# Kernel optimization log

Measured on AMD Instinct MI355X. Metric: run time of the kernel, lower is better.

Reference implementation:

```python
import jax, jax.numpy as jnp
import numpy as np

B, J, D, T = 4096, 22, 3, 50  # batch, joints, xyz dims, seq_len
N = J * D                     # 66 channels
LW = 3                        # local_window
TAU = 5.0
EPS = 1e-5


def _chain_adj_mask(n):
    m = np.zeros((n, n), dtype=np.float32)
    for i in range(n - 1):
        m[i, i + 1] = 1.0
        m[i + 1, i] = 1.0
    return m


def _band_mask(t, w):
    i = np.arange(t)
    return (np.abs(i[:, None] - i[None, :]) <= w).astype(np.float32)


def setup_inputs() -> dict:
    key = jax.random.key(0)
    ks = jax.random.split(key, 9)
    x = jax.random.normal(ks[0], (B, N, T), dtype=jnp.float32)
    adj = jnp.eye(J, dtype=jnp.float32) + 0.1 * jax.random.normal(ks[1], (J, J), dtype=jnp.float32)
    adj_t = 0.1 * jax.random.normal(ks[2], (T, T), dtype=jnp.float32)
    adj_jc = 0.1 * jax.random.normal(ks[3], (J, D, D), dtype=jnp.float32)
    adj_tj = 0.1 * jax.random.normal(ks[4], (N, T, T), dtype=jnp.float32)
    mlp = jax.random.normal(ks[5], (T, 4), dtype=jnp.float32)
    w_update = 1e-2 * jax.random.normal(ks[6], (T, T), dtype=jnp.float32)
    b_update = jnp.zeros((T,), dtype=jnp.float32)
    alpha = jnp.ones((1, N, 1), dtype=jnp.float32)
    beta = jnp.zeros((1, N, 1), dtype=jnp.float32)
    adj_mask = jnp.asarray(_chain_adj_mask(J))
    traj_mask = jnp.asarray(_band_mask(T, LW))
    u = jax.random.uniform(ks[7], (B, 4), minval=1e-6, maxval=1.0 - 1e-6, dtype=jnp.float32)
    gumbels = -jnp.log(-jnp.log(u))
    return {"x": x, "adj": adj, "adj_t": adj_t, "adj_jc": adj_jc, "adj_tj": adj_tj,
            "mlp": mlp, "w_update": w_update, "b_update": b_update,
            "alpha": alpha, "beta": beta, "adj_mask": adj_mask,
            "traj_mask": traj_mask, "gumbels": gumbels}


def reference(x, adj, adj_t, adj_jc, adj_tj, mlp, w_update, b_update,
              alpha, beta, adj_mask, traj_mask, gumbels):
    xr = x.reshape(B, J, D, T)
    # spatial GC: masked joint-joint adjacency
    x1 = jnp.einsum('vj,bjct->bvct', adj * adj_mask, xr).reshape(B, N, T)
    # temporal GC: banded time-time adjacency shared over channels
    x2 = jnp.einsum('ft,bnt->bnf', adj_t * traj_mask, x)
    # joint-channel GC: per-joint 3x3 channel mixing
    x3 = jnp.einsum('jkc,bjct->bjkt', adj_jc, xr).reshape(B, N, T)
    # spatio-temporal GC: per-channel banded time-time adjacency
    x4 = jnp.einsum('nft,bnt->bnf', adj_tj * traj_mask[None], x)
    # gate: mean-pool over channels -> [B,T] @ [T,4], hard gumbel-softmax
    prob = x.mean(axis=1) @ mlp
    y = jax.nn.softmax((prob + gumbels) / TAU, axis=-1)
    y_hard = jax.nn.one_hot(jnp.argmax(y, axis=-1), 4, dtype=y.dtype)
    gate = y_hard + y - jax.lax.stop_gradient(y)  # straight-through
    # option 0 is zeros, so only options 1..3 contribute
    x_ = (gate[:, 1, None, None] * x2
          + gate[:, 2, None, None] * x3
          + gate[:, 3, None, None] * x4)
    # update linear along time axis
    x_ = (x1 + x_) @ w_update.T + b_update
    # spatial LayerNorm over channel axis
    mean = x_.mean(axis=1, keepdims=True)
    var = ((x_ - mean) ** 2).mean(axis=1, keepdims=True)
    x_ = (x_ - mean) / jnp.sqrt(var + EPS) * alpha + beta
    return x + x_
```

## Files before the change

kernel.cpp:

```cpp
#include <hip/hip_runtime.h>


typedef __attribute__((ext_vector_type(8))) short short8_t;
typedef __attribute__((ext_vector_type(4))) float f32x4_t;

__device__ __forceinline__ unsigned short f2bf(float f) {
    unsigned u = __float_as_uint(f);
    u += 0x7fffu + ((u >> 16) & 1u);
    return (unsigned short)(u >> 16);
}
__device__ __forceinline__ float bf2f(unsigned us) {
    return __uint_as_float(us << 16);
}

#define XLD(nn, tt) (*(const uint2*)((const char*)xbf + (((((nn) << 6) + (tt)) << 1) ^ (((nn) & 7) << 4))))

__global__ __launch_bounds__(256) void pack_kernel(
    const float* __restrict__ adj_t,
    const float* __restrict__ adj_tj,
    unsigned short* __restrict__ ws)
{
    int i = blockIdx.x * 256 + threadIdx.x;
    if (i < 400) {
        int f = i >> 3, j = i & 7;
        int tt = f - 3 + j;
        float v = (j < 7 && tt >= 0 && tt < 50) ? adj_t[f * 50 + tt] : 0.f;
        ws[i] = f2bf(v);
    } else if (i < 26800) {
        int e = i - 400;
        int nf = e >> 3, j = e & 7;
        int f = nf % 50;
        int tt = f - 3 + j;
        float v = (j < 7 && tt >= 0 && tt < 50) ? adj_tj[(size_t)nf * 50 + tt] : 0.f;
        ws[i] = f2bf(v);
    }
}

__global__ __launch_bounds__(256, 2) void dyn_kernel(
    const float* __restrict__ x,
    const float* __restrict__ adj,
    const float* __restrict__ adj_t,
    const float* __restrict__ adj_jc,
    const float* __restrict__ adj_tj,
    const float* __restrict__ mlp,
    const float* __restrict__ w_update,
    const float* __restrict__ alpha,
    const float* __restrict__ beta,
    const float* __restrict__ gumbels,
    const unsigned short* __restrict__ wpack,
    int packed,
    float* __restrict__ out)
{
    __shared__ unsigned short xbf[66 * 64];
    __shared__ float wsum[16];
    __shared__ float as[66], bs[66];

    const int b    = blockIdx.x;
    const int tid  = threadIdx.x;
    const int lane = tid & 63;
    const int wv   = tid >> 6;
    const int li   = lane & 15;
    const int lq   = lane >> 4;
    const int f    = wv * 16 + li;
    const float* __restrict__ xb = x + (size_t)b * 3300;

    const float4 gv = *(const float4*)(gumbels + (size_t)b * 4);

    int sn[4], st0[4], sv[4];
    float cwm[4], cwp[4];
    #pragma unroll
    for (int r = 0; r < 4; ++r) {
        int i = tid + (r << 8);
        if (r == 3 && i > 857) i = 857;
        int n = i / 13, q = i - n * 13;
        sn[r] = n; st0[r] = q * 4;
        int v = n / 3; sv[r] = v;
        cwm[r] = (v > 0)  ? adj[v * 22 + v - 1] : 0.f;
        cwp[r] = (v < 21) ? adj[v * 22 + v + 1] : 0.f;
    }

    short8_t bfrag0, bfrag1;
    #pragma unroll
    for (int j = 0; j < 8; ++j) {
        int k0 = 8 * lq + j;
        int k1 = 32 + 8 * lq + j;
        float v0 = (f < 50) ? w_update[f * 50 + k0] : 0.f;
        float v1 = (f < 50 && k1 < 50) ? w_update[f * 50 + k1] : 0.f;
        bfrag0[j] = (short)f2bf(v0);
        bfrag1[j] = (short)f2bf(v1);
    }

    for (int i = tid; i < 198; i += 256) {
        int n = i / 3, p = i - n * 3;
        int t0 = 52 + p * 4;
        int byteoff = ((n * 64 + t0) * 2) ^ ((n & 7) << 4);
        uint2 z2; z2.x = 0u; z2.y = 0u;
        *(uint2*)((char*)xbf + byteoff) = z2;
    }
    if (tid < 66) { as[tid] = alpha[tid]; bs[tid] = beta[tid]; }

    float2 xa[4], xc[4];
    #pragma unroll
    for (int r = 0; r < 4; ++r) {
        int off = sn[r] * 50 + st0[r];
        xa[r] = *(const float2*)(xb + off);
        int off2 = off + 2; if (off2 > 3298) off2 = 3298;
        xc[r] = *(const float2*)(xb + off2);
    }
    float4 pl = {0.f, 0.f, 0.f, 0.f};
    const float4* __restrict__ mlp4 = (const float4*)mlp;
    #pragma unroll
    for (int r = 0; r < 4; ++r) {
        int n = sn[r], t0 = st0[r];
        bool full = (t0 < 48);
        float v0 = xa[r].x, v1 = xa[r].y;
        float v2 = full ? xc[r].x : 0.f;
        float v3 = full ? xc[r].y : 0.f;
        float4 m0 = mlp4[t0], m1 = mlp4[t0 + 1];
        int i2 = t0 + 2; if (i2 > 49) i2 = 49;
        int i3 = t0 + 3; if (i3 > 49) i3 = 49;
        float4 m2 = mlp4[i2], m3 = mlp4[i3];
        if (r < 3 || tid < 90) {
            pl.x += v0 * m0.x + v1 * m1.x + v2 * m2.x + v3 * m3.x;
            pl.y += v0 * m0.y + v1 * m1.y + v2 * m2.y + v3 * m3.y;
            pl.z += v0 * m0.z + v1 * m1.z + v2 * m2.z + v3 * m3.z;
            pl.w += v0 * m0.w + v1 * m1.w + v2 * m2.w + v3 * m3.w;
        }
        uint2 pk;
        pk.x = (unsigned)f2bf(v0) | ((unsigned)f2bf(v1) << 16);
        pk.y = (unsigned)f2bf(v2) | ((unsigned)f2bf(v3) << 16);
        *(uint2*)((char*)xbf + (((n * 64 + t0) * 2) ^ ((n & 7) << 4))) = pk;
    }
    #pragma unroll
    for (int d = 1; d < 64; d <<= 1) {
        pl.x += __shfl_xor(pl.x, d, 64);
        pl.y += __shfl_xor(pl.y, d, 64);
        pl.z += __shfl_xor(pl.z, d, 64);
        pl.w += __shfl_xor(pl.w, d, 64);
    }
    if (lane == 0) *(float4*)&wsum[wv * 4] = pl;
    __syncthreads();

    int g;
    {
        float4 s0 = *(const float4*)&wsum[0],  s1 = *(const float4*)&wsum[4];
        float4 s2 = *(const float4*)&wsum[8],  s3 = *(const float4*)&wsum[12];
        const float inv = 1.0f / 66.0f;
        float l0 = (s0.x + s1.x + s2.x + s3.x) * inv + gv.x;
        float l1 = (s0.y + s1.y + s2.y + s3.y) * inv + gv.y;
        float l2 = (s0.z + s1.z + s2.z + s3.z) * inv + gv.z;
        float l3 = (s0.w + s1.w + s2.w + s3.w) * inv + gv.w;
        g = 0; float bv = l0;
        if (l1 > bv) { bv = l1; g = 1; }
        if (l2 > bv) { bv = l2; g = 2; }
        if (l3 > bv) { bv = l3; g = 3; }
    }

    uint2 zpk[4];
    if (g == 1 || g == 3) {
        uint4 w0[4], w1[4];
        auto loadrows = [&](int r, uint4* dst) {
            if (packed) {
                const uint4* wt4 = (const uint4*)
                    ((g == 1) ? wpack : wpack + 400 + (size_t)sn[r] * 400);
                #pragma unroll
                for (int k = 0; k < 4; ++k) {
                    int ff = st0[r] + k; if (ff > 49) ff = 49;
                    dst[k] = wt4[ff];
                }
            } else {
                const float* rb = (g == 1) ? adj_t : (adj_tj + (size_t)sn[r] * 2500);
                #pragma unroll
                for (int k = 0; k < 4; ++k) {
                    int ff = st0[r] + k; if (ff > 49) ff = 49;
                    float w[8];
                    #pragma unroll
                    for (int j = 0; j < 8; ++j) {
                        int tt = ff - 3 + j;
                        w[j] = (j < 7 && tt >= 0 && tt < 50) ? rb[ff * 50 + tt] : 0.f;
                    }
                    uint4 u;
                    u.x = (unsigned)f2bf(w[0]) | ((unsigned)f2bf(w[1]) << 16);
                    u.y = (unsigned)f2bf(w[2]) | ((unsigned)f2bf(w[3]) << 16);
                    u.z = (unsigned)f2bf(w[4]) | ((unsigned)f2bf(w[5]) << 16);
                    u.w = (unsigned)f2bf(w[6]) | ((unsigned)f2bf(w[7]) << 16);
                    dst[k] = u;
                }
            }
        };
        loadrows(0, w0);
        #pragma unroll
        for (int r = 0; r < 4; ++r) {
            uint4* wcur = (r & 1) ? w1 : w0;
            uint4* wnxt = (r & 1) ? w0 : w1;
            if (r < 3) loadrows(r + 1, wnxt);
            int n = sn[r], t0 = st0[r];
            uint2 pm = {0u, 0u}, pp = {0u, 0u};
            if (n >= 3)  pm = XLD(n - 3, t0);
            if (n <= 62) pp = XLD(n + 3, t0);
            float acc0 = cwm[r] * bf2f(pm.x & 0xffff) + cwp[r] * bf2f(pp.x & 0xffff);
            float acc1 = cwm[r] * bf2f(pm.x >> 16)    + cwp[r] * bf2f(pp.x >> 16);
            float acc2 = cwm[r] * bf2f(pm.y & 0xffff) + cwp[r] * bf2f(pp.y & 0xffff);
            float acc3 = cwm[r] * bf2f(pm.y >> 16)    + cwp[r] * bf2f(pp.y >> 16);
            float xr[12];
            if (t0 >= 4) {
                uint2 p0 = XLD(n, t0 - 4);
                xr[0] = bf2f(p0.x & 0xffff); xr[1] = bf2f(p0.x >> 16);
                xr[2] = bf2f(p0.y & 0xffff); xr[3] = bf2f(p0.y >> 16);
            } else { xr[0] = 0.f; xr[1] = 0.f; xr[2] = 0.f; xr[3] = 0.f; }
            {
                uint2 p1 = XLD(n, t0);
                xr[4] = bf2f(p1.x & 0xffff); xr[5] = bf2f(p1.x >> 16);
                xr[6] = bf2f(p1.y & 0xffff); xr[7] = bf2f(p1.y >> 16);
            }
            {
                uint2 p2 = XLD(n, t0 + 4);
                xr[8]  = bf2f(p2.x & 0xffff); xr[9]  = bf2f(p2.x >> 16);
                xr[10] = bf2f(p2.y & 0xffff); xr[11] = bf2f(p2.y >> 16);
            }
            #pragma unroll
            for (int j = 0; j < 4; ++j) {
                int ff = t0 + j;
                if (ff < 50) {
                    uint4 u = wcur[j];
                    float a = bf2f(u.x & 0xffff) * xr[j + 1]
                            + bf2f(u.x >> 16)    * xr[j + 2]
                            + bf2f(u.y & 0xffff) * xr[j + 3]
                            + bf2f(u.y >> 16)    * xr[j + 4]
                            + bf2f(u.z & 0xffff) * xr[j + 5]
                            + bf2f(u.z >> 16)    * xr[j + 6]
                            + bf2f(u.w & 0xffff) * xr[j + 7];
                    if (j == 0) acc0 += a; else if (j == 1) acc1 += a;
                    else if (j == 2) acc2 += a; else acc3 += a;
                }
            }
            zpk[r].x = (unsigned)f2bf(acc0) | ((unsigned)f2bf(acc1) << 16);
            zpk[r].y = (unsigned)f2bf(acc2) | ((unsigned)f2bf(acc3) << 16);
        }
    } else {
        #pragma unroll
        for (int r = 0; r < 4; ++r) {
            int n = sn[r], t0 = st0[r], v = sv[r];
            uint2 pm = {0u, 0u}, pp = {0u, 0u};
            if (n >= 3)  pm = XLD(n - 3, t0);
            if (n <= 62) pp = XLD(n + 3, t0);
            float acc0 = cwm[r] * bf2f(pm.x & 0xffff) + cwp[r] * bf2f(pp.x & 0xffff);
            float acc1 = cwm[r] * bf2f(pm.x >> 16)    + cwp[r] * bf2f(pp.x >> 16);
            float acc2 = cwm[r] * bf2f(pm.y & 0xffff) + cwp[r] * bf2f(pp.y & 0xffff);
            float acc3 = cwm[r] * bf2f(pm.y >> 16)    + cwp[r] * bf2f(pp.y >> 16);
            if (g == 2) {
                int c = n - v * 3;
                const float* ajc = adj_jc + (size_t)(v * 3 + c) * 3;
                #pragma unroll
                for (int cc = 0; cc < 3; ++cc) {
                    float w = ajc[cc];
                    uint2 p = XLD(v * 3 + cc, t0);
                    acc0 += w * bf2f(p.x & 0xffff); acc1 += w * bf2f(p.x >> 16);
                    acc2 += w * bf2f(p.y & 0xffff); acc3 += w * bf2f(p.y >> 16);
                }
            }
            zpk[r].x = (unsigned)f2bf(acc0) | ((unsigned)f2bf(acc1) << 16);
            zpk[r].y = (unsigned)f2bf(acc2) | ((unsigned)f2bf(acc3) << 16);
        }
    }
    __syncthreads();

    #pragma unroll
    for (int r = 0; r < 4; ++r) {
        int n = sn[r], t0 = st0[r];
        *(uint2*)((char*)xbf + (((n * 64 + t0) * 2) ^ ((n & 7) << 4))) = zpk[r];
    }
    __syncthreads();

    f32x4_t dacc[5];
    #pragma unroll
    for (int mt = 0; mt < 5; ++mt) dacc[mt] = (f32x4_t){0.f, 0.f, 0.f, 0.f};

    #pragma unroll
    for (int ks = 0; ks < 2; ++ks) {
        short8_t bfrag = ks ? bfrag1 : bfrag0;
        #pragma unroll
        for (int mt = 0; mt < 5; ++mt) {
            int m = mt * 16 + li;
            short8_t afrag = {0, 0, 0, 0, 0, 0, 0, 0};
            if (m < 66)
                afrag = *(const short8_t*)((const char*)xbf + (((m * 64 + 8 * lq + 32 * ks) * 2) ^ ((m & 7) << 4)));
            dacc[mt] = __builtin_amdgcn_mfma_f32_16x16x32_bf16(afrag, bfrag, dacc[mt], 0, 0, 0);
        }
    }

    float S = 0.f, SS = 0.f;
    #pragma unroll
    for (int mt = 0; mt < 5; ++mt) {
        #pragma unroll
        for (int r = 0; r < 4; ++r) {
            int m = mt * 16 + lq * 4 + r;
            if (mt < 4 || m < 66) { float d = dacc[mt][r]; S += d; SS += d * d; }
        }
    }
    S  += __shfl_xor(S, 16, 64);  S  += __shfl_xor(S, 32, 64);
    SS += __shfl_xor(SS, 16, 64); SS += __shfl_xor(SS, 32, 64);
    const float mean = S * (1.f / 66.f);
    const float var  = SS * (1.f / 66.f) - mean * mean;
    const float rstd = rsqrtf(var + 1e-5f);

    if (f < 50) {
        float* __restrict__ ob = out + (size_t)b * 3300;
        #pragma unroll
        for (int mt = 0; mt < 5; ++mt) {
            #pragma unroll
            for (int r = 0; r < 4; ++r) {
                int m = mt * 16 + lq * 4 + r;
                if (mt < 4 || m < 66) {
                    float xv = xb[m * 50 + f];
                    float xn = (dacc[mt][r] - mean) * rstd;
                    ob[m * 50 + f] = xv + xn * as[m] + bs[m];
                }
            }
        }
    }
}

extern "C" void kernel_launch(void* const* d_in, const int* in_sizes, int n_in,
                              void* d_out, int out_size, void* d_ws, size_t ws_size,
                              hipStream_t stream) {
    (void)in_sizes; (void)n_in; (void)out_size;
    const float* x        = (const float*)d_in[0];
    const float* adj      = (const float*)d_in[1];
    const float* adj_t    = (const float*)d_in[2];
    const float* adj_jc   = (const float*)d_in[3];
    const float* adj_tj   = (const float*)d_in[4];
    const float* mlp      = (const float*)d_in[5];
    const float* w_update = (const float*)d_in[6];
    const float* alpha    = (const float*)d_in[8];
    const float* beta     = (const float*)d_in[9];
    const float* gumbels  = (const float*)d_in[12];

    const size_t pack_bytes = (size_t)26800 * sizeof(unsigned short);
    int packed = (d_ws != nullptr && ws_size >= pack_bytes) ? 1 : 0;
    unsigned short* ws = (unsigned short*)d_ws;
    if (packed)
        pack_kernel<<<105, 256, 0, stream>>>(adj_t, adj_tj, ws);

    dyn_kernel<<<4096, 256, 0, stream>>>(x, adj, adj_t, adj_jc, adj_tj, mlp,
                                         w_update, alpha, beta, gumbels,
                                         ws, packed, (float*)d_out);
}
```

Before: 61.33 us.

## Map one batch element per wavefront, removing block barriers, and pre-pack w_update

Work is restructured so each wave of a 128-thread block handles a whole batch element with its own LDS tile. Block-wide __syncthreads and the shared-memory reduction for the gate become wave-local shuffles and wave barriers. Each wave now runs 14 elementwise iterations and 4 MFMA output tiles instead of one, with w_update pre-packed to bf16 in workspace. This removes cross-wave synchronisation at the cost of more serial work per wave and higher register pressure from the zpk[14] array.

```diff
diff --git a/kernel.cpp b/kernel.cpp
--- a/kernel.cpp
+++ b/kernel.cpp
@@ -12,12 +12,20 @@
 __device__ __forceinline__ float bf2f(unsigned us) {
     return __uint_as_float(us << 16);
 }
-
-#define XLD(nn, tt) (*(const uint2*)((const char*)xbf + (((((nn) << 6) + (tt)) << 1) ^ (((nn) & 7) << 4))))
+__device__ __forceinline__ uint2 qld(const unsigned short* base, int n, int t) {
+    return *(const uint2*)((const char*)base + (((n * 64 + t) * 2) ^ ((n & 7) << 4)));
+}
+__device__ __forceinline__ void qst(unsigned short* base, int n, int t, uint2 v) {
+    *(uint2*)((char*)base + (((n * 64 + t) * 2) ^ ((n & 7) << 4))) = v;
+}
+
+#define WS_W_SOFF 26800
+#define WS_SHORTS (26800 + 4096)
 
 __global__ __launch_bounds__(256) void pack_kernel(
     const float* __restrict__ adj_t,
     const float* __restrict__ adj_tj,
+    const float* __restrict__ w_update,
     unsigned short* __restrict__ ws)
 {
     int i = blockIdx.x * 256 + threadIdx.x;
@@ -33,10 +41,15 @@
         int tt = f - 3 + j;
         float v = (j < 7 && tt >= 0 && tt < 50) ? adj_tj[(size_t)nf * 50 + tt] : 0.f;
         ws[i] = f2bf(v);
-    }
-}
-
-__global__ __launch_bounds__(256, 2) void dyn_kernel(
+    } else if (i < WS_SHORTS) {
+        int e = i - WS_W_SOFF;
+        int fo = e >> 6, k = e & 63;
+        float v = (fo < 50 && k < 50) ? w_update[fo * 50 + k] : 0.f;
+        ws[i] = f2bf(v);
+    }
+}
+
+__global__ __launch_bounds__(128, 4) void dyn_kernel(
     const float* __restrict__ x,
     const float* __restrict__ adj,
     const float* __restrict__ adj_t,
@@ -51,76 +64,49 @@
     int packed,
     float* __restrict__ out)
 {
-    __shared__ unsigned short xbf[66 * 64];
-    __shared__ float wsum[16];
+    __shared__ unsigned short xls[2][66 * 64];
     __shared__ float as[66], bs[66];
 
-    const int b    = blockIdx.x;
     const int tid  = threadIdx.x;
     const int lane = tid & 63;
-    const int wv   = tid >> 6;
+    const int w    = tid >> 6;
     const int li   = lane & 15;
     const int lq   = lane >> 4;
-    const int f    = wv * 16 + li;
+    const int b    = blockIdx.x * 2 + w;
+    unsigned short* __restrict__ xw = xls[w];
     const float* __restrict__ xb = x + (size_t)b * 3300;
 
     const float4 gv = *(const float4*)(gumbels + (size_t)b * 4);
 
-    int sn[4], st0[4], sv[4];
-    float cwm[4], cwp[4];
-    #pragma unroll
-    for (int r = 0; r < 4; ++r) {
-        int i = tid + (r << 8);
-        if (r == 3 && i > 857) i = 857;
-        int n = i / 13, q = i - n * 13;
-        sn[r] = n; st0[r] = q * 4;
-        int v = n / 3; sv[r] = v;
-        cwm[r] = (v > 0)  ? adj[v * 22 + v - 1] : 0.f;
-        cwp[r] = (v < 21) ? adj[v * 22 + v + 1] : 0.f;
-    }
-
-    short8_t bfrag0, bfrag1;
-    #pragma unroll
-    for (int j = 0; j < 8; ++j) {
-        int k0 = 8 * lq + j;
-        int k1 = 32 + 8 * lq + j;
-        float v0 = (f < 50) ? w_update[f * 50 + k0] : 0.f;
-        float v1 = (f < 50 && k1 < 50) ? w_update[f * 50 + k1] : 0.f;
-        bfrag0[j] = (short)f2bf(v0);
-        bfrag1[j] = (short)f2bf(v1);
-    }
-
-    for (int i = tid; i < 198; i += 256) {
+    as[lane] = alpha[lane]; bs[lane] = beta[lane];
+    if (lane < 2) { as[64 + lane] = alpha[64 + lane]; bs[64 + lane] = beta[64 + lane]; }
+
+    for (int i = lane; i < 198; i += 64) {
         int n = i / 3, p = i - n * 3;
-        int t0 = 52 + p * 4;
-        int byteoff = ((n * 64 + t0) * 2) ^ ((n & 7) << 4);
         uint2 z2; z2.x = 0u; z2.y = 0u;
-        *(uint2*)((char*)xbf + byteoff) = z2;
-    }
-    if (tid < 66) { as[tid] = alpha[tid]; bs[tid] = beta[tid]; }
-
-    float2 xa[4], xc[4];
-    #pragma unroll
-    for (int r = 0; r < 4; ++r) {
-        int off = sn[r] * 50 + st0[r];
-        xa[r] = *(const float2*)(xb + off);
-        int off2 = off + 2; if (off2 > 3298) off2 = 3298;
-        xc[r] = *(const float2*)(xb + off2);
-    }
+        qst(xw, n, 52 + p * 4, z2);
+    }
+
     float4 pl = {0.f, 0.f, 0.f, 0.f};
     const float4* __restrict__ mlp4 = (const float4*)mlp;
-    #pragma unroll
-    for (int r = 0; r < 4; ++r) {
-        int n = sn[r], t0 = st0[r];
+    for (int s = 0; s < 14; ++s) {
+        int i = s * 64 + lane;
+        bool valid = (s < 13) | (lane < 26);
+        int ic = valid ? i : 857;
+        int n = ic / 13, q = ic - n * 13;
+        int t0 = q * 4;
+        int off = n * 50 + t0;
+        float2 a = *(const float2*)(xb + off);
+        int off2 = off + 2; if (off2 > 3298) off2 = 3298;
+        float2 c2 = *(const float2*)(xb + off2);
         bool full = (t0 < 48);
-        float v0 = xa[r].x, v1 = xa[r].y;
-        float v2 = full ? xc[r].x : 0.f;
-        float v3 = full ? xc[r].y : 0.f;
+        float v0 = a.x, v1 = a.y;
+        float v2 = full ? c2.x : 0.f, v3 = full ? c2.y : 0.f;
         float4 m0 = mlp4[t0], m1 = mlp4[t0 + 1];
         int i2 = t0 + 2; if (i2 > 49) i2 = 49;
         int i3 = t0 + 3; if (i3 > 49) i3 = 49;
         float4 m2 = mlp4[i2], m3 = mlp4[i3];
-        if (r < 3 || tid < 90) {
+        if (valid) {
             pl.x += v0 * m0.x + v1 * m1.x + v2 * m2.x + v3 * m3.x;
             pl.y += v0 * m0.y + v1 * m1.y + v2 * m2.y + v3 * m3.y;
             pl.z += v0 * m0.z + v1 * m1.z + v2 * m2.z + v3 * m3.z;
@@ -129,7 +115,7 @@
         uint2 pk;
         pk.x = (unsigned)f2bf(v0) | ((unsigned)f2bf(v1) << 16);
         pk.y = (unsigned)f2bf(v2) | ((unsigned)f2bf(v3) << 16);
-        *(uint2*)((char*)xbf + (((n * 64 + t0) * 2) ^ ((n & 7) << 4))) = pk;
+        qst(xw, n, t0, pk);
     }
     #pragma unroll
     for (int d = 1; d < 64; d <<= 1) {
@@ -138,83 +124,78 @@
         pl.z += __shfl_xor(pl.z, d, 64);
         pl.w += __shfl_xor(pl.w, d, 64);
     }
-    if (lane == 0) *(float4*)&wsum[wv * 4] = pl;
-    __syncthreads();
-
     int g;
     {
-        float4 s0 = *(const float4*)&wsum[0],  s1 = *(const float4*)&wsum[4];
-        float4 s2 = *(const float4*)&wsum[8],  s3 = *(const float4*)&wsum[12];
         const float inv = 1.0f / 66.0f;
-        float l0 = (s0.x + s1.x + s2.x + s3.x) * inv + gv.x;
-        float l1 = (s0.y + s1.y + s2.y + s3.y) * inv + gv.y;
-        float l2 = (s0.z + s1.z + s2.z + s3.z) * inv + gv.z;
-        float l3 = (s0.w + s1.w + s2.w + s3.w) * inv + gv.w;
+        float l0 = pl.x * inv + gv.x, l1 = pl.y * inv + gv.y;
+        float l2 = pl.z * inv + gv.z, l3 = pl.w * inv + gv.w;
         g = 0; float bv = l0;
         if (l1 > bv) { bv = l1; g = 1; }
         if (l2 > bv) { bv = l2; g = 2; }
         if (l3 > bv) { bv = l3; g = 3; }
     }
-
-    uint2 zpk[4];
+    __builtin_amdgcn_wave_barrier();
+
+    uint2 zpk[14];
     if (g == 1 || g == 3) {
-        uint4 w0[4], w1[4];
-        auto loadrows = [&](int r, uint4* dst) {
+        #pragma unroll
+        for (int s = 0; s < 14; ++s) {
+            int i = s * 64 + lane;
+            bool valid = (s < 13) | (lane < 26);
+            int ic = valid ? i : 857;
+            int n = ic / 13, q = ic - n * 13;
+            int t0 = q * 4;
+            uint4 wr[4];
             if (packed) {
                 const uint4* wt4 = (const uint4*)
-                    ((g == 1) ? wpack : wpack + 400 + (size_t)sn[r] * 400);
+                    ((g == 1) ? wpack : wpack + 400 + (size_t)n * 400);
                 #pragma unroll
-                for (int k = 0; k < 4; ++k) {
-                    int ff = st0[r] + k; if (ff > 49) ff = 49;
-                    dst[k] = wt4[ff];
+                for (int kk = 0; kk < 4; ++kk) {
+                    int ff = t0 + kk; if (ff > 49) ff = 49;
+                    wr[kk] = wt4[ff];
                 }
             } else {
-                const float* rb = (g == 1) ? adj_t : (adj_tj + (size_t)sn[r] * 2500);
+                const float* rb = (g == 1) ? adj_t : (adj_tj + (size_t)n * 2500);
                 #pragma unroll
-                for (int k = 0; k < 4; ++k) {
-                    int ff = st0[r] + k; if (ff > 49) ff = 49;
-                    float w[8];
+                for (int kk = 0; kk < 4; ++kk) {
+                    int ff = t0 + kk; if (ff > 49) ff = 49;
+                    float ww[8];
                     #pragma unroll
                     for (int j = 0; j < 8; ++j) {
                         int tt = ff - 3 + j;
-                        w[j] = (j < 7 && tt >= 0 && tt < 50) ? rb[ff * 50 + tt] : 0.f;
+                        ww[j] = (j < 7 && tt >= 0 && tt < 50) ? rb[ff * 50 + tt] : 0.f;
                     }
                     uint4 u;
-                    u.x = (unsigned)f2bf(w[0]) | ((unsigned)f2bf(w[1]) << 16);
-                    u.y = (unsigned)f2bf(w[2]) | ((unsigned)f2bf(w[3]) << 16);
-                    u.z = (unsigned)f2bf(w[4]) | ((unsigned)f2bf(w[5]) << 16);
-                    u.w = (unsigned)f2bf(w[6]) | ((unsigned)f2bf(w[7]) << 16);
-                    dst[k] = u;
-                }
-            }
-        };
-        loadrows(0, w0);
-        #pragma unroll
-        for (int r = 0; r < 4; ++r) {
-            uint4* wcur = (r & 1) ? w1 : w0;
-            uint4* wnxt = (r & 1) ? w0 : w1;
-            if (r < 3) loadrows(r + 1, wnxt);
-            int n = sn[r], t0 = st0[r];
+                    u.x = (unsigned)f2bf(ww[0]) | ((unsigned)f2bf(ww[1]) << 16);
+                    u.y = (unsigned)f2bf(ww[2]) | ((unsigned)f2bf(ww[3]) << 16);
+                    u.z = (unsigned)f2bf(ww[4]) | ((unsigned)f2bf(ww[5]) << 16);
+                    u.w = (unsigned)f2bf(ww[6]) | ((unsigned)f2bf(ww[7]) << 16);
+                    wr[kk] = u;
+                }
+            }
+            int vv = n / 3;
+            float cwm = (vv > 0)  ? adj[vv * 22 + vv - 1] : 0.f;
+            float cwp = (vv < 21) ? adj[vv * 22 + vv + 1] : 0.f;
             uint2 pm = {0u, 0u}, pp = {0u, 0u};
-            if (n >= 3)  pm = XLD(n - 3, t0);
-            if (n <= 62) pp = XLD(n + 3, t0);
-            float acc0 = cwm[r] * bf2f(pm.x & 0xffff) + cwp[r] * bf2f(pp.x & 0xffff);
-            float acc1 = cwm[r] * bf2f(pm.x >> 16)    + cwp[r] * bf2f(pp.x >> 16);
-            float acc2 = cwm[r] * bf2f(pm.y & 0xffff) + cwp[r] * bf2f(pp.y & 0xffff);
-            float acc3 = cwm[r] * bf2f(pm.y >> 16)    + cwp[r] * bf2f(pp.y >> 16);
+            if (n >= 3)  pm = qld(xw, n - 3, t0);
+            if (n <= 62) pp = qld(xw, n + 3, t0);
+            float acc0 = cwm * bf2f(pm.x & 0xffff) + cwp * bf2f(pp.x & 0xffff);
+            float acc1 = cwm * bf2f(pm.x >> 16)    + cwp * bf2f(pp.x >> 16);
+            float acc2 = cwm * bf2f(pm.y & 0xffff) + cwp * bf2f(pp.y & 0xffff);
+            float acc3 = cwm * bf2f(pm.y >> 16)    + cwp * bf2f(pp.y >> 16);
             float xr[12];
             if (t0 >= 4) {
-                uint2 p0 = XLD(n, t0 - 4);
+                uint2 p0 = qld(xw, n, t0 - 4);
                 xr[0] = bf2f(p0.x & 0xffff); xr[1] = bf2f(p0.x >> 16);
                 xr[2] = bf2f(p0.y & 0xffff); xr[3] = bf2f(p0.y >> 16);
             } else { xr[0] = 0.f; xr[1] = 0.f; xr[2] = 0.f; xr[3] = 0.f; }
             {
-                uint2 p1 = XLD(n, t0);
+                uint2 p1 = qld(xw, n, t0);
                 xr[4] = bf2f(p1.x & 0xffff); xr[5] = bf2f(p1.x >> 16);
                 xr[6] = bf2f(p1.y & 0xffff); xr[7] = bf2f(p1.y >> 16);
             }
             {
-                uint2 p2 = XLD(n, t0 + 4);
+                uint2 p2 = qld(xw, n, t0 + 4);
                 xr[8]  = bf2f(p2.x & 0xffff); xr[9]  = bf2f(p2.x >> 16);
                 xr[10] = bf2f(p2.y & 0xffff); xr[11] = bf2f(p2.y >> 16);
             }
@@ -222,7 +203,7 @@
             for (int j = 0; j < 4; ++j) {
                 int ff = t0 + j;
                 if (ff < 50) {
-                    uint4 u = wcur[j];
+                    uint4 u = wr[j];
                     float a = bf2f(u.x & 0xffff) * xr[j + 1]
                             + bf2f(u.x >> 16)    * xr[j + 2]
                             + bf2f(u.y & 0xffff) * xr[j + 3]
@@ -234,87 +215,116 @@
                     else if (j == 2) acc2 += a; else acc3 += a;
                 }
             }
-            zpk[r].x = (unsigned)f2bf(acc0) | ((unsigned)f2bf(acc1) << 16);
-            zpk[r].y = (unsigned)f2bf(acc2) | ((unsigned)f2bf(acc3) << 16);
+            zpk[s].x = (unsigned)f2bf(acc0) | ((unsigned)f2bf(acc1) << 16);
+            zpk[s].y = (unsigned)f2bf(acc2) | ((unsigned)f2bf(acc3) << 16);
+            __builtin_amdgcn_sched_barrier(0);
         }
     } else {
         #pragma unroll
-        for (int r = 0; r < 4; ++r) {
-            int n = sn[r], t0 = st0[r], v = sv[r];
+        for (int s = 0; s < 14; ++s) {
+            int i = s * 64 + lane;
+            bool valid = (s < 13) | (lane < 26);
+            int ic = valid ? i : 857;
+            int n = ic / 13, q = ic - n * 13;
+            int t0 = q * 4;
+            int vv = n / 3;
+            float cwm = (vv > 0)  ? adj[vv * 22 + vv - 1] : 0.f;
+            float cwp = (vv < 21) ? adj[vv * 22 + vv + 1] : 0.f;
             uint2 pm = {0u, 0u}, pp = {0u, 0u};
-            if (n >= 3)  pm = XLD(n - 3, t0);
-            if (n <= 62) pp = XLD(n + 3, t0);
-            float acc0 = cwm[r] * bf2f(pm.x & 0xffff) + cwp[r] * bf2f(pp.x & 0xffff);
-            float acc1 = cwm[r] * bf2f(pm.x >> 16)    + cwp[r] * bf2f(pp.x >> 16);
-            float acc2 = cwm[r] * bf2f(pm.y & 0xffff) + cwp[r] * bf2f(pp.y & 0xffff);
-            float acc3 = cwm[r] * bf2f(pm.y >> 16)    + cwp[r] * bf2f(pp.y >> 16);
+            if (n >= 3)  pm = qld(xw, n - 3, t0);
+            if (n <= 62) pp = qld(xw, n + 3, t0);
+            float acc0 = cwm * bf2f(pm.x & 0xffff) + cwp * bf2f(pp.x & 0xffff);
+            float acc1 = cwm * bf2f(pm.x >> 16)    + cwp * bf2f(pp.x >> 16);
+            float acc2 = cwm * bf2f(pm.y & 0xffff) + cwp * bf2f(pp.y & 0xffff);
+            float acc3 = cwm * bf2f(pm.y >> 16)    + cwp * bf2f(pp.y >> 16);
             if (g == 2) {
-                int c = n - v * 3;
-                const float* ajc = adj_jc + (size_t)(v * 3 + c) * 3;
+                const float* ajc = adj_jc + (size_t)n * 3;
                 #pragma unroll
                 for (int cc = 0; cc < 3; ++cc) {
-                    float w = ajc[cc];
-                    uint2 p = XLD(v * 3 + cc, t0);
-                    acc0 += w * bf2f(p.x & 0xffff); acc1 += w * bf2f(p.x >> 16);
-                    acc2 += w * bf2f(p.y & 0xffff); acc3 += w * bf2f(p.y >> 16);
-                }
-            }
-            zpk[r].x = (unsigned)f2bf(acc0) | ((unsigned)f2bf(acc1) << 16);
-            zpk[r].y = (unsigned)f2bf(acc2) | ((unsigned)f2bf(acc3) << 16);
-        }
-    }
-    __syncthreads();
+                    float ww = ajc[cc];
+                    uint2 p = qld(xw, vv * 3 + cc, t0);
+                    acc0 += ww * bf2f(p.x & 0xffff); acc1 += ww * bf2f(p.x >> 16);
+                    acc2 += ww * bf2f(p.y & 0xffff); acc3 += ww * bf2f(p.y >> 16);
+                }
+            }
+            zpk[s].x = (unsigned)f2bf(acc0) | ((unsigned)f2bf(acc1) << 16);
+            zpk[s].y = (unsigned)f2bf(acc2) | ((unsigned)f2bf(acc3) << 16);
+            __builtin_amdgcn_sched_barrier(0);
+        }
+    }
+    __builtin_amdgcn_wave_barrier();
 
     #pragma unroll
-    for (int r = 0; r < 4; ++r) {
-        int n = sn[r], t0 = st0[r];
-        *(uint2*)((char*)xbf + (((n * 64 + t0) * 2) ^ ((n & 7) << 4))) = zpk[r];
-    }
-    __syncthreads();
-
-    f32x4_t dacc[5];
-    #pragma unroll
-    for (int mt = 0; mt < 5; ++mt) dacc[mt] = (f32x4_t){0.f, 0.f, 0.f, 0.f};
-
-    #pragma unroll
-    for (int ks = 0; ks < 2; ++ks) {
-        short8_t bfrag = ks ? bfrag1 : bfrag0;
-        #pragma unroll
-        for (int mt = 0; mt < 5; ++mt) {
-            int m = mt * 16 + li;
-            short8_t afrag = {0, 0, 0, 0, 0, 0, 0, 0};
-            if (m < 66)
-                afrag = *(const short8_t*)((const char*)xbf + (((m * 64 + 8 * lq + 32 * ks) * 2) ^ ((m & 7) << 4)));
-            dacc[mt] = __builtin_amdgcn_mfma_f32_16x16x32_bf16(afrag, bfrag, dacc[mt], 0, 0, 0);
-        }
-    }
-
-    float S = 0.f, SS = 0.f;
-    #pragma unroll
-    for (int mt = 0; mt < 5; ++mt) {
-        #pragma unroll
-        for (int r = 0; r < 4; ++r) {
-            int m = mt * 16 + lq * 4 + r;
-            if (mt < 4 || m < 66) { float d = dacc[mt][r]; S += d; SS += d * d; }
-        }
-    }
-    S  += __shfl_xor(S, 16, 64);  S  += __shfl_xor(S, 32, 64);
-    SS += __shfl_xor(SS, 16, 64); SS += __shfl_xor(SS, 32, 64);
-    const float mean = S * (1.f / 66.f);
-    const float var  = SS * (1.f / 66.f) - mean * mean;
-    const float rstd = rsqrtf(var + 1e-5f);
-
-    if (f < 50) {
-        float* __restrict__ ob = out + (size_t)b * 3300;
+    for (int s = 0; s < 14; ++s) {
+        int i = s * 64 + lane;
+        bool valid = (s < 13) | (lane < 26);
+        int ic = valid ? i : 857;
+        int n = ic / 13, q = ic - n * 13;
+        qst(xw, n, q * 4, zpk[s]);
+    }
+    __builtin_amdgcn_wave_barrier();
+
+    float* __restrict__ ob = out + (size_t)b * 3300;
+    for (int ft = 0; ft < 4; ++ft) {
+        int fp = ft * 16 + li;
+        short8_t wf0, wf1;
+        if (packed) {
+            const unsigned short* wwb = wpack + WS_W_SOFF;
+            wf0 = *(const short8_t*)(wwb + fp * 64 + 8 * lq);
+            wf1 = *(const short8_t*)(wwb + fp * 64 + 8 * lq + 32);
+        } else {
+            #pragma unroll
+            for (int j = 0; j < 8; ++j) {
+                int ka = 8 * lq + j, kb = 32 + 8 * lq + j;
+                float va = (fp < 50) ? w_update[fp * 50 + ka] : 0.f;
+                float vb = (fp < 50 && kb < 50) ? w_update[fp * 50 + kb] : 0.f;
+                wf0[j] = (short)f2bf(va);
+                wf1[j] = (short)f2bf(vb);
+            }
+        }
+        f32x4_t dacc[5];
+        #pragma unroll
+        for (int mt = 0; mt < 5; ++mt) dacc[mt] = (f32x4_t){0.f, 0.f, 0.f, 0.f};
+        #pragma unroll
+        for (int ks = 0; ks < 2; ++ks) {
+            short8_t bfrag = ks ? wf1 : wf0;
+            #pragma unroll
+            for (int mt = 0; mt < 5; ++mt) {
+                int m = mt * 16 + li;
+                short8_t afrag = {0, 0, 0, 0, 0, 0, 0, 0};
+                if (m < 66)
+                    afrag = *(const short8_t*)((const char*)xw +
+                        (((m * 64 + 8 * lq + 32 * ks) * 2) ^ ((m & 7) << 4)));
+                dacc[mt] = __builtin_amdgcn_mfma_f32_16x16x32_bf16(afrag, bfrag, dacc[mt], 0, 0, 0);
+            }
+        }
+
+        float S = 0.f, SS = 0.f;
         #pragma unroll
         for (int mt = 0; mt < 5; ++mt) {
             #pragma unroll
             for (int r = 0; r < 4; ++r) {
                 int m = mt * 16 + lq * 4 + r;
-                if (mt < 4 || m < 66) {
-                    float xv = xb[m * 50 + f];
-                    float xn = (dacc[mt][r] - mean) * rstd;
-                    ob[m * 50 + f] = xv + xn * as[m] + bs[m];
+                if (mt < 4 || m < 66) { float d = dacc[mt][r]; S += d; SS += d * d; }
+            }
+        }
+        S  += __shfl_xor(S, 16, 64);  S  += __shfl_xor(S, 32, 64);
+        SS += __shfl_xor(SS, 16, 64); SS += __shfl_xor(SS, 32, 64);
+        const float mean = S * (1.f / 66.f);
+        const float var  = SS * (1.f / 66.f) - mean * mean;
+        const float rstd = rsqrtf(var + 1e-5f);
+
+        if (fp < 50) {
+            #pragma unroll
+            for (int mt = 0; mt < 5; ++mt) {
+                #pragma unroll
+                for (int r = 0; r < 4; ++r) {
+                    int m = mt * 16 + lq * 4 + r;
+                    if (mt < 4 || m < 66) {
+                        float xv = xb[m * 50 + fp];
+                        float xn = (dacc[mt][r] - mean) * rstd;
+                        ob[m * 50 + fp] = xv + xn * as[m] + bs[m];
+                    }
                 }
             }
         }
@@ -336,13 +346,13 @@
     const float* beta     = (const float*)d_in[9];
     const float* gumbels  = (const float*)d_in[12];
 
-    const size_t pack_bytes = (size_t)26800 * sizeof(unsigned short);
+    const size_t pack_bytes = (size_t)WS_SHORTS * sizeof(unsigned short);
     int packed = (d_ws != nullptr && ws_size >= pack_bytes) ? 1 : 0;
     unsigned short* ws = (unsigned short*)d_ws;
     if (packed)
-        pack_kernel<<<105, 256, 0, stream>>>(adj_t, adj_tj, ws);
-
-    dyn_kernel<<<4096, 256, 0, stream>>>(x, adj, adj_t, adj_jc, adj_tj, mlp,
+        pack_kernel<<<(WS_SHORTS + 255) / 256, 256, 0, stream>>>(adj_t, adj_tj, w_update, ws);
+
+    dyn_kernel<<<2048, 128, 0, stream>>>(x, adj, adj_t, adj_jc, adj_tj, mlp,
                                          w_update, alpha, beta, gumbels,
                                          ws, packed, (float*)d_out);
 }
```

Result: slower. 94.47 us (+54.0%).
